# Optimization experiments

Measured on AMD Instinct MI355X. Metric: run time of the kernel, lower is better.

Reference implementation:

```python
import jax, jax.numpy as jnp
import numpy as np


def _dct_matrix():
    # orthonormal 8x8 DCT-II matrix, matches cv2.dct
    k = jnp.arange(8.0)[:, None]
    n = jnp.arange(8.0)[None, :]
    D = jnp.sqrt(2.0 / 8.0) * jnp.cos(jnp.pi * (2.0 * n + 1.0) * k / 16.0)
    return D.at[0, :].multiply(1.0 / jnp.sqrt(2.0))


def setup_inputs() -> dict:
    key = jax.random.key(0)
    k = jax.random.split(key, 8)
    C, R = 64, 32  # num_channels, num_channels // reduction_ratio
    return {
        "x": jax.random.uniform(k[0], (256, 256, 3), dtype=jnp.float32),
        "fc1_w": jax.random.normal(k[1], (R, C), dtype=jnp.float32) * 0.1,
        "fc1_b": jax.random.normal(k[2], (R,), dtype=jnp.float32) * 0.1,
        "fc2_w": jax.random.normal(k[3], (C, R), dtype=jnp.float32) * 0.1,
        "fc2_b": jax.random.normal(k[4], (C,), dtype=jnp.float32) * 0.1,
        "sse_w": jax.random.normal(k[5], (C,), dtype=jnp.float32) * 0.1,
        "sse_b": jax.random.normal(k[6], (), dtype=jnp.float32) * 0.1,
        "bs": 64,
    }


def reference(x, fc1_w, fc1_b, fc2_w, fc2_b, sse_w, sse_b, bs):
    D = _dct_matrix().astype(x.dtype)
    # se_dct: channel 0 -> 8x8 blocks (row-major block order) -> per-block 2D DCT
    img = x[:, :, 0]                                           # (256,256)
    blocks = img.reshape(32, 8, 32, 8).transpose(1, 3, 0, 2).reshape(8, 8, 1024)
    dct = jnp.einsum('ik,klc,jl->ijc', D, blocks, D)           # (8,8,1024)
    # se_fre: fre[:,:,i*8+j] = dct[i,j,:].reshape(32,32).T
    fre = dct.reshape(64, 32, 32).transpose(2, 1, 0)           # (32,32,64)
    # ChannelSpatialSELayer on (64,32,32); batch copies are identical so compute once
    feat = fre.transpose(2, 0, 1)                              # (64,32,32)
    sq = feat.mean(axis=(1, 2))                                # (64,)
    h = jax.nn.relu(sq @ fc1_w.T + fc1_b)
    scale_c = jax.nn.sigmoid(h @ fc2_w.T + fc2_b)              # (64,)
    cse = feat * scale_c[:, None, None]
    spatial = jax.nn.sigmoid(jnp.einsum('c,chw->hw', sse_w, feat) + sse_b)
    sse = feat * spatial[None, :, :]
    y = jnp.maximum(cse, sse)                                  # (64,32,32)
    # se_ifre: array[ch//8, ch%8, :] = y_hwc[:,:,ch].T.flatten()
    y_hwc = y.transpose(1, 2, 0)                               # (32,32,64)
    arr = y_hwc.transpose(2, 1, 0).reshape(8, 8, 1024)
    # se_idct: per-block 2D inverse DCT, reassemble 256x256
    idct = jnp.einsum('ki,klc,lj->ijc', D, arr, D)             # (8,8,1024)
    out2d = idct.reshape(8, 8, 32, 32).transpose(2, 0, 3, 1).reshape(256, 256)
    # se_2dto3d + final se_transpose: repeat to 3 channels, tile batch
    return jnp.broadcast_to(out2d[None, None, :, :], (bs, 3, 256, 256))
```

## Files before the change

kernel.cpp:

```cpp
#include <hip/hip_runtime.h>
#include <hip/hip_bf16.h>
#include <math.h>

__device__ __forceinline__ float dctD(int k, int n) {
    const float c[9] = {1.0f, 0.98078528040323043f, 0.92387953251128674f,
                        0.83146961230254524f, 0.70710678118654752f,
                        0.55557023301960218f, 0.38268343236508977f,
                        0.19509032201612825f, 0.0f};
    int m = ((2 * n + 1) * k) & 31;
    float s = 1.0f;
    if (m > 16) m = 32 - m;
    if (m > 8) { m = 16 - m; s = -1.0f; }
    float scale = (k == 0) ? 0.35355339059327373f : 0.5f;
    return scale * s * c[m];
}

__device__ __forceinline__ float sigmoidf(float a) {
    return 1.0f / (1.0f + expf(-a));
}

#define WS_FEAT   0
#define WS_GPART  65536

__global__ __launch_bounds__(256) void dct_kernel(const float* __restrict__ x,
                                                  float* __restrict__ feat,
                                                  float* __restrict__ gpart) {
    __shared__ float Ds[64];
    __shared__ float xs[32][65];
    __shared__ float red[4][64];
    int tid = threadIdx.x;
    if (tid < 64) Ds[tid] = dctD(tid >> 3, tid & 7);
    int b = tid & 31, r = tid >> 5;
    int t = blockIdx.x * 32 + b;
    int br = t >> 5, bc = t & 31;

    const float4* xrow4 = (const float4*)(x + ((br * 8 + r) * 256 + bc * 8) * 3);
    float4 v0 = xrow4[0], v1 = xrow4[1], v2 = xrow4[2];
    float4 v3 = xrow4[3], v4 = xrow4[4], v5 = xrow4[5];
    xs[b][r * 8 + 0] = v0.x;  xs[b][r * 8 + 1] = v0.w;
    xs[b][r * 8 + 2] = v1.z;  xs[b][r * 8 + 3] = v2.y;
    xs[b][r * 8 + 4] = v3.x;  xs[b][r * 8 + 5] = v3.w;
    xs[b][r * 8 + 6] = v4.z;  xs[b][r * 8 + 7] = v5.y;
    __syncthreads();

    float tr[8];
    #pragma unroll
    for (int l = 0; l < 8; l++) tr[l] = 0.f;
    #pragma unroll
    for (int k = 0; k < 8; k++) {
        float d = Ds[r * 8 + k];
        #pragma unroll
        for (int l = 0; l < 8; l++) tr[l] += d * xs[b][k * 8 + l];
    }
    float o[8];
    #pragma unroll
    for (int j = 0; j < 8; j++) {
        float s = 0.f;
        #pragma unroll
        for (int l = 0; l < 8; l++) s += tr[l] * Ds[j * 8 + l];
        o[j] = s;
        feat[(r * 8 + j) * 1024 + t] = s;
    }
    __syncthreads();
    #pragma unroll
    for (int j = 0; j < 8; j++) xs[b][r * 8 + j] = o[j];
    __syncthreads();

    int c = tid & 63, qg = tid >> 6;
    float s = 0.f;
    #pragma unroll
    for (int bb = 0; bb < 8; bb++) s += xs[qg * 8 + bb][c];
    red[qg][c] = s;
    __syncthreads();
    if (tid < 64)
        gpart[blockIdx.x * 64 + tid] =
            red[0][tid] + red[1][tid] + red[2][tid] + red[3][tid];
}

__global__ __launch_bounds__(256) void idct_bcast_kernel(const float* __restrict__ feat,
                                                         const float* __restrict__ gpart,
                                                         const float* __restrict__ fc1_w,
                                                         const float* __restrict__ fc1_b,
                                                         const float* __restrict__ fc2_w,
                                                         const float* __restrict__ fc2_b,
                                                         const float* __restrict__ sse_w,
                                                         const float* __restrict__ sse_b,
                                                         float* __restrict__ out,
                                                         int nimg) {
    __shared__ float Ds[64], sw[64], sq[64], sc[64], h[32], spat[32];
    __shared__ float redp[8][33];
    __shared__ float tmls[32][65];
    __shared__ float otile[2048];
    int tid = threadIdx.x;
    int tg = blockIdx.x & 31;
    int ig = blockIdx.x >> 5;

    if (tid < 64) {
        Ds[tid] = dctD(tid >> 3, tid & 7);
        sw[tid] = sse_w[tid];
        float s = 0.f;
        #pragma unroll
        for (int w = 0; w < 32; w++) s += gpart[w * 64 + tid];
        sq[tid] = s * (1.0f / 1024.0f);
    }
    __syncthreads();
    if (tid < 32) {
        float a = fc1_b[tid];
        #pragma unroll 8
        for (int cc = 0; cc < 64; cc++) a += sq[cc] * fc1_w[tid * 64 + cc];
        h[tid] = fmaxf(a, 0.f);
    }
    __syncthreads();
    if (tid < 64) {
        float a = fc2_b[tid];
        #pragma unroll 8
        for (int rr = 0; rr < 32; rr++) a += h[rr] * fc2_w[tid * 32 + rr];
        sc[tid] = sigmoidf(a);
    }

    int b = tid & 31, r = tid >> 5;
    int t = tg * 32 + b;

    float gr[8];
    #pragma unroll
    for (int l = 0; l < 8; l++) gr[l] = feat[(r * 8 + l) * 1024 + t];
    float sp = 0.f;
    #pragma unroll
    for (int l = 0; l < 8; l++) sp += sw[r * 8 + l] * gr[l];
    redp[r][b] = sp;
    __syncthreads();
    if (tid < 32) {
        float a = sse_b[0];
        #pragma unroll
        for (int rr = 0; rr < 8; rr++) a += redp[rr][tid];
        spat[tid] = sigmoidf(a);
    }
    __syncthreads();

    float spb = spat[b];
    float tm[8];
    #pragma unroll
    for (int j = 0; j < 8; j++) tm[j] = 0.f;
    #pragma unroll
    for (int l = 0; l < 8; l++) {
        float v = gr[l];
        float y = fmaxf(v * sc[r * 8 + l], v * spb);
        #pragma unroll
        for (int j = 0; j < 8; j++) tm[j] += y * Ds[l * 8 + j];
    }
    #pragma unroll
    for (int j = 0; j < 8; j++) tmls[b][r * 8 + j] = tm[j];
    __syncthreads();

    float o[8];
    #pragma unroll
    for (int j = 0; j < 8; j++) o[j] = 0.f;
    #pragma unroll
    for (int k = 0; k < 8; k++) {
        float d = Ds[k * 8 + r];
        #pragma unroll
        for (int j = 0; j < 8; j++) o[j] += d * tmls[b][k * 8 + j];
    }
    #pragma unroll
    for (int j = 0; j < 8; j++) otile[r * 256 + b * 8 + j] = o[j];
    __syncthreads();

    const float4* src = (const float4*)otile;
    float4 w0 = src[tid];
    float4 w1 = src[tid + 256];
    #pragma unroll
    for (int m = 0; m < 6; m++) {
        int img = ig * 6 + m;
        if (img < nimg) {
            float4* dst = (float4*)(out + (size_t)img * 65536 + tg * 2048);
            dst[tid] = w0;
            dst[tid + 256] = w1;
        }
    }
}

extern "C" void kernel_launch(void* const* d_in, const int* in_sizes, int n_in,
                              void* d_out, int out_size, void* d_ws, size_t ws_size,
                              hipStream_t stream) {
    const float* x     = (const float*)d_in[0];
    const float* fc1_w = (const float*)d_in[1];
    const float* fc1_b = (const float*)d_in[2];
    const float* fc2_w = (const float*)d_in[3];
    const float* fc2_b = (const float*)d_in[4];
    const float* sse_w = (const float*)d_in[5];
    const float* sse_b = (const float*)d_in[6];
    float* ws = (float*)d_ws;
    float* feat  = ws + WS_FEAT;
    float* gpart = ws + WS_GPART;
    float* out = (float*)d_out;
    int nimg = out_size / 65536;

    dct_kernel<<<32, 256, 0, stream>>>(x, feat, gpart);
    idct_bcast_kernel<<<1024, 256, 0, stream>>>(feat, gpart, fc1_w, fc1_b,
                                                fc2_w, fc2_b, sse_w, sse_b,
                                                out, nimg);
}
```

Measured before the change: 93.86 us.

## Compute output plane once, then broadcast with nontemporal stores

```diff
diff --git a/kernel.cpp b/kernel.cpp
--- a/kernel.cpp
+++ b/kernel.cpp
@@ -1,6 +1,7 @@
 #include <hip/hip_runtime.h>
-#include <hip/hip_bf16.h>
 #include <math.h>
+
+typedef float f32x4 __attribute__((ext_vector_type(4)));
 
 __device__ __forceinline__ float dctD(int k, int n) {
     const float c[9] = {1.0f, 0.98078528040323043f, 0.92387953251128674f,
@@ -21,6 +22,7 @@
 
 #define WS_FEAT   0
 #define WS_GPART  65536
+#define WS_PLANE  67584
 
 __global__ __launch_bounds__(256) void dct_kernel(const float* __restrict__ x,
                                                   float* __restrict__ feat,
@@ -77,23 +79,20 @@
             red[0][tid] + red[1][tid] + red[2][tid] + red[3][tid];
 }
 
-__global__ __launch_bounds__(256) void idct_bcast_kernel(const float* __restrict__ feat,
-                                                         const float* __restrict__ gpart,
-                                                         const float* __restrict__ fc1_w,
-                                                         const float* __restrict__ fc1_b,
-                                                         const float* __restrict__ fc2_w,
-                                                         const float* __restrict__ fc2_b,
-                                                         const float* __restrict__ sse_w,
-                                                         const float* __restrict__ sse_b,
-                                                         float* __restrict__ out,
-                                                         int nimg) {
+__global__ __launch_bounds__(256) void plane_kernel(const float* __restrict__ feat,
+                                                    const float* __restrict__ gpart,
+                                                    const float* __restrict__ fc1_w,
+                                                    const float* __restrict__ fc1_b,
+                                                    const float* __restrict__ fc2_w,
+                                                    const float* __restrict__ fc2_b,
+                                                    const float* __restrict__ sse_w,
+                                                    const float* __restrict__ sse_b,
+                                                    float* __restrict__ plane) {
     __shared__ float Ds[64], sw[64], sq[64], sc[64], h[32], spat[32];
     __shared__ float redp[8][33];
     __shared__ float tmls[32][65];
-    __shared__ float otile[2048];
     int tid = threadIdx.x;
-    int tg = blockIdx.x & 31;
-    int ig = blockIdx.x >> 5;
+    int tg = blockIdx.x;
 
     if (tid < 64) {
         Ds[tid] = dctD(tid >> 3, tid & 7);
@@ -161,20 +160,28 @@
         #pragma unroll
         for (int j = 0; j < 8; j++) o[j] += d * tmls[b][k * 8 + j];
     }
-    #pragma unroll
-    for (int j = 0; j < 8; j++) otile[r * 256 + b * 8 + j] = o[j];
-    __syncthreads();
-
-    const float4* src = (const float4*)otile;
-    float4 w0 = src[tid];
-    float4 w1 = src[tid + 256];
+    float4* dst = (float4*)(plane + tg * 2048 + r * 256 + b * 8);
+    dst[0] = make_float4(o[0], o[1], o[2], o[3]);
+    dst[1] = make_float4(o[4], o[5], o[6], o[7]);
+}
+
+__global__ __launch_bounds__(256) void bcast_kernel(const float* __restrict__ plane,
+                                                    float* __restrict__ out,
+                                                    int nimg) {
+    int tid = threadIdx.x;
+    int tg = blockIdx.x & 31;
+    int ig = blockIdx.x >> 5;
+
+    const f32x4* src = (const f32x4*)(plane + tg * 2048);
+    f32x4 w0 = src[tid];
+    f32x4 w1 = src[tid + 256];
     #pragma unroll
     for (int m = 0; m < 6; m++) {
         int img = ig * 6 + m;
         if (img < nimg) {
-            float4* dst = (float4*)(out + (size_t)img * 65536 + tg * 2048);
-            dst[tid] = w0;
-            dst[tid + 256] = w1;
+            f32x4* dst = (f32x4*)(out + (size_t)img * 65536 + tg * 2048);
+            __builtin_nontemporal_store(w0, dst + tid);
+            __builtin_nontemporal_store(w1, dst + tid + 256);
         }
     }
 }
@@ -192,11 +199,13 @@
     float* ws = (float*)d_ws;
     float* feat  = ws + WS_FEAT;
     float* gpart = ws + WS_GPART;
+    float* plane = ws + WS_PLANE;
     float* out = (float*)d_out;
     int nimg = out_size / 65536;
 
     dct_kernel<<<32, 256, 0, stream>>>(x, feat, gpart);
-    idct_bcast_kernel<<<1024, 256, 0, stream>>>(feat, gpart, fc1_w, fc1_b,
-                                                fc2_w, fc2_b, sse_w, sse_b,
-                                                out, nimg);
-}
+    plane_kernel<<<32, 256, 0, stream>>>(feat, gpart, fc1_w, fc1_b,
+                                         fc2_w, fc2_b, sse_w, sse_b, plane);
+    int ngrp = (nimg + 5) / 6;
+    bcast_kernel<<<ngrp * 32, 256, 0, stream>>>(plane, out, nimg);
+}
```

Result: no change. 93.44 us (-0.4%).
